# Kernel tuning notes

Measured on AMD Instinct MI355X. Metric: run time of the kernel, lower is better.

Reference implementation:

```python
import jax, jax.numpy as jnp
import numpy as np

P = 6
CUTOFF = 1.0
N_BASIS = 8
AVG_NEIGH = 16.0
NUM_LAYERS = 2
N, E, MUL, H, F = 8192, 131072, 16, 256, 16


def envelope(d):
    # polynomial cutoff u(x) with p=6 (NequIP/Allegro style)
    x = d / CUTOFF
    p = float(P)
    u = (1.0 - (p + 1.0) * (p + 2.0) / 2.0 * x ** P
         + p * (p + 2.0) * x ** (P + 1)
         - p * (p + 1.0) / 2.0 * x ** (P + 2))
    return jnp.where(x < 1.0, u, 0.0)


def bessel(d):
    k = jnp.arange(1, N_BASIS + 1, dtype=d.dtype)
    return jnp.sqrt(2.0 / CUTOFF) * jnp.sin(k[None, :] * jnp.pi * d[:, None] / CUTOFF) / d[:, None]


def sph_harm(u):
    # real spherical harmonics, ell=0..3, component normalization -> [E,16]
    x, y, z = u[:, 0], u[:, 1], u[:, 2]
    s3 = 3.0 ** 0.5
    s5 = 5.0 ** 0.5
    s15 = 15.0 ** 0.5
    s7 = 7.0 ** 0.5
    c33 = (35.0 / 8.0) ** 0.5
    c32 = 105.0 ** 0.5
    c31 = (21.0 / 8.0) ** 0.5
    one = jnp.ones_like(x)
    comps = [
        one,
        s3 * x, s3 * y, s3 * z,
        s15 * x * y, s15 * y * z, 0.5 * s5 * (3.0 * z * z - 1.0), s15 * x * z, 0.5 * s15 * (x * x - y * y),
        c33 * y * (3.0 * x * x - y * y), c32 * x * y * z, c31 * y * (5.0 * z * z - 1.0),
        0.5 * s7 * (5.0 * z ** 3 - 3.0 * z), c31 * x * (5.0 * z * z - 1.0),
        0.5 * c32 * z * (x * x - y * y), c33 * x * (x * x - 3.0 * y * y),
    ]
    return jnp.stack(comps, axis=1)


def setup_inputs() -> dict:
    key = jax.random.key(0)
    ks = jax.random.split(key, 16)
    dirs = jax.random.normal(ks[0], (E, 3), dtype=jnp.float32)
    dirs = dirs / jnp.linalg.norm(dirs, axis=1, keepdims=True)
    r = jax.random.uniform(ks[1], (E, 1), minval=0.05, maxval=0.95, dtype=jnp.float32)
    vectors = dirs * r
    node_attrs = 0.5 * jax.random.normal(ks[2], (N, F), dtype=jnp.float32)
    senders = jax.random.randint(ks[3], (E,), 0, N, dtype=jnp.int32)
    receivers = jax.random.randint(ks[4], (E,), 0, N, dtype=jnp.int32)

    def gl(k, shape):
        fan_in = shape[-2] if len(shape) >= 2 else 1
        return jax.random.normal(k, shape, dtype=jnp.float32) / jnp.sqrt(float(fan_in))

    return {
        'node_attrs': node_attrs, 'vectors': vectors,
        'senders': senders, 'receivers': receivers,
        'W_e0': gl(ks[5], (N_BASIS + 2 * F, H)), 'b_e0': jnp.zeros((H,), jnp.float32),
        'W_e1': gl(ks[6], (H, H)), 'b_e1': jnp.zeros((H,), jnp.float32),
        'W_v0': gl(ks[7], (H, MUL)),
        'W_lw': gl(ks[8], (NUM_LAYERS, H, MUL)),
        'W_lsh': gl(ks[9], (NUM_LAYERS, 16, 16)),
        'W_ly1': gl(ks[10], (NUM_LAYERS, H + MUL, H)), 'b_ly1': jnp.zeros((NUM_LAYERS, H), jnp.float32),
        'W_ly2': gl(ks[11], (NUM_LAYERS, H, H)), 'b_ly2': jnp.zeros((NUM_LAYERS, H), jnp.float32),
        'W_out': gl(ks[12], (H, 1)),
    }


def reference(node_attrs, vectors, senders, receivers, W_e0, b_e0, W_e1, b_e1, W_v0,
              W_lw, W_lsh, W_ly1, b_ly1, W_ly2, b_ly2, W_out):
    n_nodes = node_attrs.shape[0]
    inv = 1.0 / jnp.sqrt(AVG_NEIGH)
    d = jnp.linalg.norm(vectors, axis=1)                      # [E]
    u = envelope(d)                                           # [E]
    # edge embedding: radial basis + gathered endpoint attrs
    x = jnp.concatenate([bessel(d), node_attrs[senders], node_attrs[receivers]], axis=1)
    x = jax.nn.silu(x @ W_e0 + b_e0)
    x = jax.nn.silu(x @ W_e1 + b_e1)
    x = u[:, None] * x                                        # [E,H]
    Y = sph_harm(vectors / d[:, None])                        # [E,16]
    V = (x @ W_v0)[:, :, None] * Y[:, None, :]                # [E,MUL,16]
    for l in range(NUM_LAYERS):
        w = x @ W_lw[l]                                       # [E,MUL]
        wY = jax.ops.segment_sum(w[:, :, None] * Y[:, None, :], senders, num_segments=n_nodes) * inv
        wY = wY[senders]                                      # [E,MUL,16] gather back
        VV = wY * V                                           # per-edge equivariant product
        V = jnp.einsum('emi,ij->emj', VV, W_lsh[l])
        h = jnp.concatenate([x, VV[:, :, 0]], axis=1)         # scalar (l=0) channel feedback
        y = jax.nn.silu(h @ W_ly1[l] + b_ly1[l])
        y = jax.nn.silu(y @ W_ly2[l] + b_ly2[l])
        x = (x + u[:, None] * y) / jnp.sqrt(2.0)
    edge_out = (x @ W_out) * u[:, None]                       # [E,1]
    node_out = jax.ops.segment_sum(edge_out, receivers, num_segments=n_nodes) * inv
    return node_out                                           # [N,1]
```

## Files before the change

### kernel.cpp

```cpp
#include <hip/hip_runtime.h>
#include <hip/hip_bf16.h>
#include <math.h>

#define H 256
#define F 16
#define MUL 16
#define NB 8
#define LROW 296
#define YROW 264

typedef short bf16x8 __attribute__((ext_vector_type(8)));
typedef short bf16x4 __attribute__((ext_vector_type(4)));
typedef float f32x4 __attribute__((ext_vector_type(4)));
#define MFMA_B16(a, b, c) __builtin_amdgcn_mfma_f32_16x16x32_bf16(a, b, c, 0, 0, 0)

__device__ __forceinline__ float bf2f(__hip_bfloat16 x) { return __bfloat162float(x); }
__device__ __forceinline__ float silu(float x)
{
    return x * __builtin_amdgcn_rcpf(1.f + __expf(-x));
}
__device__ __forceinline__ short f2bs(float x)
{
    __hip_bfloat16 h = __float2bfloat16(x);
    short s; __builtin_memcpy(&s, &h, 2); return s;
}
__device__ __forceinline__ float bs2f(short s)
{
    __hip_bfloat16 h; __builtin_memcpy(&h, &s, 2); return __bfloat162float(h);
}
__device__ __forceinline__ float rawld(const void* p, int flag, size_t o)
{
    return flag ? ((const float*)p)[o] : bf2f(((const __hip_bfloat16*)p)[o]);
}

__global__ __launch_bounds__(256) void k_sniff(const void* vec, int* flag,
                                               int* cnt, int N)
{
    __shared__ int bad;
    int tid = threadIdx.x;
    if (tid == 0) bad = 0;
    __syncthreads();
    const __hip_bfloat16* hp = (const __hip_bfloat16*)vec;
    for (int i = tid; i < 1024; i += 256) {
        float f = bf2f(hp[i]);
        if (!(isfinite(f) && fabsf(f) <= 1.0f)) bad = 1;
    }
    for (int i = tid; i < N; i += 256) cnt[i] = 0;
    __syncthreads();
    if (tid == 0) *flag = bad;
}

struct ConvArgs {
    const void* src[7];
    float* dst[7];
    int cum[8];
};
__global__ __launch_bounds__(256) void k_conv_all(ConvArgs a, const int* __restrict__ flag,
                                                  const int* __restrict__ snd,
                                                  int* __restrict__ cnt, int E)
{
    int gid = blockIdx.x * 256 + threadIdx.x;
    if (gid < E) atomicAdd(&cnt[snd[gid]], 1);
    if (gid >= a.cum[7]) return;
    int k = 0;
    while (gid >= a.cum[k + 1]) k++;
    int i = gid - a.cum[k];
    a.dst[k][i] = rawld(a.src[k], *flag, i);
}

struct SwzArgs {
    const void* src[10];
    __hip_bfloat16* dst[10];
    int K[10], Nc[10], cum[11];
    size_t soff[10];
};
__global__ __launch_bounds__(256) void k_swz_all(SwzArgs a, const int* __restrict__ flag)
{
    int gid = blockIdx.x * 256 + threadIdx.x;
    if (gid >= a.cum[10]) return;
    int fl = *flag;
    int j = 0;
    while (gid >= a.cum[j + 1]) j++;
    int idx = gid - a.cum[j];
    int kk = idx & 31;
    int n = (idx >> 5) % a.Nc[j];
    int kt = idx / (32 * a.Nc[j]);
    int k = kt * 32 + kk;
    float v = 0.f;
    if (j == 9) {
        if (n == 0 && k < a.K[j]) v = rawld(a.src[j], fl, a.soff[j] + k);
    } else if (k < a.K[j]) {
        v = rawld(a.src[j], fl, a.soff[j] + (size_t)k * a.Nc[j] + n);
    }
    a.dst[j][idx] = __float2bfloat16(v);
}

__global__ __launch_bounds__(1024) void k_scan(const int* __restrict__ cnt,
                                               int* __restrict__ off,
                                               int* __restrict__ cur, int N)
{
    __shared__ int sums[1024];
    int tid = threadIdx.x;
    int chunk = (N + 1023) / 1024;
    int base = tid * chunk;
    int s = 0;
    for (int i = 0; i < chunk; i++) { int idx = base + i; if (idx < N) s += cnt[idx]; }
    sums[tid] = s;
    __syncthreads();
    for (int d = 1; d < 1024; d <<= 1) {
        int v = (tid >= d) ? sums[tid - d] : 0;
        __syncthreads();
        sums[tid] += v;
        __syncthreads();
    }
    int run = (tid == 0) ? 0 : sums[tid - 1];
    for (int i = 0; i < chunk; i++) {
        int idx = base + i;
        if (idx < N) { off[idx] = run; cur[idx] = run; run += cnt[idx]; }
    }
    if (tid == 1023) off[N] = run;
}

__global__ __launch_bounds__(256) void k_cscatter(const int* __restrict__ snd,
                                                  int* __restrict__ cur,
                                                  int* __restrict__ eidx, int E)
{
    int e = blockIdx.x * 256 + threadIdx.x;
    if (e >= E) return;
    int p = atomicAdd(&cur[snd[e]], 1);
    eidx[p] = e;
}


__global__ __launch_bounds__(512, 4) void k_embed_mfma(
    const float* __restrict__ vec, const float* __restrict__ na,
    const int* __restrict__ snd, const int* __restrict__ rcv,
    const __hip_bfloat16* __restrict__ We0s, const float* __restrict__ be0,
    const __hip_bfloat16* __restrict__ We1s, const float* __restrict__ be1,
    const __hip_bfloat16* __restrict__ Wv0s, const __hip_bfloat16* __restrict__ Wlws0,
    float* __restrict__ ubuf, float* __restrict__ Ybuf,
    __hip_bfloat16* __restrict__ xb, float* __restrict__ abuf,
    float* __restrict__ wbuf)
{
    __shared__ __align__(16) __hip_bfloat16 As[64 * LROW];
    __shared__ __align__(16) __hip_bfloat16 Ys[64 * YROW];
    __shared__ float us[64];
    int tid = threadIdx.x;
    int w = tid >> 6, l = tid & 63;
    int lm = l & 15, lq = l >> 4;
    int eb = blockIdx.x * 64;

    bf16x8 w0p[2][2];
#pragma unroll
    for (int kt = 0; kt < 2; kt++)
#pragma unroll
        for (int nt = 0; nt < 2; nt++)
            w0p[kt][nt] = *(const bf16x8*)(We0s + ((size_t)(kt * 256 + w * 32 + nt * 16 + lm) * 32 + lq * 8));

    {
        int el = tid & 63;
        int part = tid >> 6;
        int ge = eb + el;
        const float SQ2 = 1.41421356237309515f;
        const float PI = 3.14159265358979323846f;
        if (part == 0) {
            float vx = vec[3 * ge + 0], vy = vec[3 * ge + 1], vz = vec[3 * ge + 2];
            float d = sqrtf(vx * vx + vy * vy + vz * vz);
            float d3 = d * d * d;
            float d6 = d3 * d3, d7 = d6 * d, d8 = d7 * d;
            float u = 1.f - 28.f * d6 + 48.f * d7 - 21.f * d8;
            u = (d < 1.f) ? u : 0.f;
            ubuf[ge] = u;
            us[el] = u;
            float invd = __builtin_amdgcn_rcpf(d);
#pragma unroll
            for (int k = 1; k <= 4; k++)
                As[el * LROW + (k - 1)] = __float2bfloat16(SQ2 * __sinf((float)k * PI * d) * invd);
        } else if (part == 4) {
            float vx = vec[3 * ge + 0], vy = vec[3 * ge + 1], vz = vec[3 * ge + 2];
            float d = sqrtf(vx * vx + vy * vy + vz * vz);
            float invd = __builtin_amdgcn_rcpf(d);
#pragma unroll
            for (int k = 5; k <= 8; k++)
                As[el * LROW + (k - 1)] = __float2bfloat16(SQ2 * __sinf((float)k * PI * d) * invd);
        } else if (part == 5) {
#pragma unroll
            for (int j = 40; j < 64; j++) As[el * LROW + j] = __float2bfloat16(0.f);
        } else if (part == 1) {
            int s = snd[ge];
#pragma unroll
            for (int j = 0; j < 16; j++)
                As[el * LROW + 8 + j] = __float2bfloat16(na[(size_t)s * F + j]);
        } else if (part == 2) {
            int r = rcv[ge];
#pragma unroll
            for (int j = 0; j < 16; j++)
                As[el * LROW + 24 + j] = __float2bfloat16(na[(size_t)r * F + j]);
        } else if (part == 3) {
            float vx = vec[3 * ge + 0], vy = vec[3 * ge + 1], vz = vec[3 * ge + 2];
            float d = sqrtf(vx * vx + vy * vy + vz * vz);
            float invd = __builtin_amdgcn_rcpf(d);
            float x = vx * invd, y = vy * invd, z = vz * invd;
            const float s3 = 1.7320508075688772f;
            const float s5 = 2.2360679774997896f;
            const float s15 = 3.8729833462074170f;
            const float s7 = 2.6457513110645907f;
            const float c33 = 2.0916500663351889f;
            const float c32 = 10.246950765959598f;
            const float c31 = 1.6201851746019651f;
            float* Yp = Ybuf + (size_t)ge * 16;
            Yp[0] = 1.f;
            Yp[1] = s3 * x;  Yp[2] = s3 * y;  Yp[3] = s3 * z;
            Yp[4] = s15 * x * y;  Yp[5] = s15 * y * z;
            Yp[6] = 0.5f * s5 * (3.f * z * z - 1.f);
            Yp[7] = s15 * x * z;
            Yp[8] = 0.5f * s15 * (x * x - y * y);
            Yp[9] = c33 * y * (3.f * x * x - y * y);
            Yp[10] = c32 * x * y * z;
            Yp[11] = c31 * y * (5.f * z * z - 1.f);
            Yp[12] = 0.5f * s7 * (5.f * z * z * z - 3.f * z);
            Yp[13] = c31 * x * (5.f * z * z - 1.f);
            Yp[14] = 0.5f * c32 * z * (x * x - y * y);
            Yp[15] = c33 * x * (x * x - 3.f * y * y);
        }
    }
    __syncthreads();

    f32x4 acc[4][2];
#pragma unroll
    for (int mt = 0; mt < 4; mt++)
#pragma unroll
        for (int nt = 0; nt < 2; nt++) acc[mt][nt] = (f32x4){0.f, 0.f, 0.f, 0.f};
#pragma unroll
    for (int kt = 0; kt < 2; kt++) {
#pragma unroll
        for (int mt = 0; mt < 4; mt++) {
            bf16x8 bx = *(const bf16x8*)(As + (mt * 16 + lm) * LROW + kt * 32 + lq * 8);
#pragma unroll
            for (int nt = 0; nt < 2; nt++) acc[mt][nt] = MFMA_B16(w0p[kt][nt], bx, acc[mt][nt]);
        }
    }
    bf16x8 w1p[2][2];
#pragma unroll
    for (int kt = 0; kt < 2; kt++)
#pragma unroll
        for (int nt = 0; nt < 2; nt++)
            w1p[kt][nt] = *(const bf16x8*)(We1s + ((size_t)(kt * 256 + w * 32 + nt * 16 + lm) * 32 + lq * 8));
#pragma unroll
    for (int nt = 0; nt < 2; nt++) {
        int cb = w * 32 + nt * 16 + lq * 4;
        f32x4 bb = *(const f32x4*)(be0 + cb);
#pragma unroll
        for (int mt = 0; mt < 4; mt++) {
            int row = mt * 16 + lm;
            bf16x4 v = {f2bs(silu(acc[mt][nt][0] + bb[0])), f2bs(silu(acc[mt][nt][1] + bb[1])),
                        f2bs(silu(acc[mt][nt][2] + bb[2])), f2bs(silu(acc[mt][nt][3] + bb[3]))};
            *(bf16x4*)(Ys + row * YROW + cb) = v;
        }
    }
    __syncthreads();

#pragma unroll
    for (int mt = 0; mt < 4; mt++)
#pragma unroll
        for (int nt = 0; nt < 2; nt++) acc[mt][nt] = (f32x4){0.f, 0.f, 0.f, 0.f};
#pragma unroll
    for (int kt = 0; kt < 8; kt++) {
        bf16x8 aw[2];
#pragma unroll
        for (int nt = 0; nt < 2; nt++)
            aw[nt] = (kt < 2) ? w1p[kt][nt]
                   : *(const bf16x8*)(We1s + ((size_t)(kt * 256 + w * 32 + nt * 16 + lm) * 32 + lq * 8));
#pragma unroll
        for (int mt = 0; mt < 4; mt++) {
            bf16x8 bx = *(const bf16x8*)(Ys + (mt * 16 + lm) * YROW + kt * 32 + lq * 8);
#pragma unroll
            for (int nt = 0; nt < 2; nt++) acc[mt][nt] = MFMA_B16(aw[nt], bx, acc[mt][nt]);
        }
    }
    const __hip_bfloat16* tw = (w < 4) ? Wv0s : Wlws0;
    bf16x8 twp[2];
#pragma unroll
    for (int kt = 0; kt < 2; kt++)
        twp[kt] = *(const bf16x8*)(tw + ((size_t)(kt * 16 + lm) * 32 + lq * 8));
#pragma unroll
    for (int nt = 0; nt < 2; nt++) {
        int cb = w * 32 + nt * 16 + lq * 4;
        f32x4 bb = *(const f32x4*)(be1 + cb);
#pragma unroll
        for (int mt = 0; mt < 4; mt++) {
            int row = mt * 16 + lm;
            float uu = us[row];
            bf16x4 v = {f2bs(silu(acc[mt][nt][0] + bb[0]) * uu),
                        f2bs(silu(acc[mt][nt][1] + bb[1]) * uu),
                        f2bs(silu(acc[mt][nt][2] + bb[2]) * uu),
                        f2bs(silu(acc[mt][nt][3] + bb[3]) * uu)};
            *(bf16x4*)(As + row * LROW + cb) = v;
            *(bf16x4*)(xb + (size_t)(eb + row) * H + cb) = v;
        }
    }
    __syncthreads();

    if (w < 4) {
        f32x4 av = (f32x4){0.f, 0.f, 0.f, 0.f};
#pragma unroll
        for (int kt = 0; kt < 8; kt++) {
            bf16x8 bx = *(const bf16x8*)(As + (w * 16 + lm) * LROW + kt * 32 + lq * 8);
            bf16x8 a_v = (kt < 2) ? twp[kt]
                       : *(const bf16x8*)(Wv0s + ((size_t)(kt * 16 + lm) * 32 + lq * 8));
            av = MFMA_B16(a_v, bx, av);
        }
        *(f32x4*)(abuf + (size_t)(eb + w * 16 + lm) * 16 + lq * 4) = av;
    } else {
        int w2 = w - 4;
        f32x4 aw2 = (f32x4){0.f, 0.f, 0.f, 0.f};
#pragma unroll
        for (int kt = 0; kt < 8; kt++) {
            bf16x8 bx = *(const bf16x8*)(As + (w2 * 16 + lm) * LROW + kt * 32 + lq * 8);
            bf16x8 a_w = (kt < 2) ? twp[kt]
                       : *(const bf16x8*)(Wlws0 + ((size_t)(kt * 16 + lm) * 32 + lq * 8));
            aw2 = MFMA_B16(a_w, bx, aw2);
        }
        *(f32x4*)(wbuf + (size_t)(eb + w2 * 16 + lm) * 16 + lq * 4) = aw2;
    }
}

__global__ __launch_bounds__(256) void k_gather0(
    const int* __restrict__ off, const int* __restrict__ eidx,
    const float* __restrict__ wbuf, const float* __restrict__ Ybuf,
    const float* __restrict__ abuf,
    float* __restrict__ wYn0, __hip_bfloat16* __restrict__ vvbuf)
{
    __shared__ float ws[4][16][17];
    __shared__ float Ysh[4][16][17];
    __shared__ float w00s[4][16];
    int tid = threadIdx.x;
    int w = tid >> 6, l = tid & 63;
    int js = l >> 4, i = l & 15;
    int n0 = blockIdx.x * 4;
    int n = n0 + w;
    int beg = off[n], end = off[n + 1];
    int o0 = off[n0], o1 = off[n0 + 1], o2 = off[n0 + 2], o3 = off[n0 + 3], o4 = off[n0 + 4];
    int m01 = max(o1 - o0, o2 - o1), m23 = max(o3 - o2, o4 - o3);
    int maxc = (max(m01, m23) + 15) >> 4;
    float acc[4] = {0.f, 0.f, 0.f, 0.f};
    for (int r = 0; r < maxc; r++) {
        int c = beg + r * 16;
        int ne = min(16, end - c);
        if (ne > 0) {
#pragma unroll
            for (int k = 0; k < 4; k++) {
                int j = js + 4 * k;
                if (j < ne) {
                    int e = eidx[c + j];
                    ws[w][j][i]  = wbuf[(size_t)e * 16 + i];
                    Ysh[w][j][i] = Ybuf[(size_t)e * 16 + i];
                }
            }
        }
        __syncthreads();
        if (ne > 0) {
            for (int j2 = 0; j2 < ne; j2++) {
                float yv = Ysh[w][j2][i];
#pragma unroll
                for (int k = 0; k < 4; k++)
                    acc[k] += ws[w][j2][js + 4 * k] * yv;
            }
        }
        __syncthreads();
    }
#pragma unroll
    for (int k = 0; k < 4; k++)
        wYn0[(size_t)n * 256 + (js + 4 * k) * 16 + i] = acc[k] * 0.25f;
    if (i == 0) {
#pragma unroll
        for (int k = 0; k < 4; k++) w00s[w][js + 4 * k] = acc[k] * 0.25f;
    }
    __syncthreads();
    float w0i = w00s[w][i];
    for (int c = beg + js; c < end; c += 4) {
        int e = eidx[c];
        float a = abuf[(size_t)e * 16 + i];
        vvbuf[(size_t)e * 16 + i] = __float2bfloat16(w0i * a);
    }
}

__global__ __launch_bounds__(256) void k_gather1(
    const int* __restrict__ off, const int* __restrict__ eidx,
    const float* __restrict__ wbuf, const float* __restrict__ Ybuf,
    const float* __restrict__ abuf,
    const float* __restrict__ wYn0, const float* __restrict__ Wlsh,
    __hip_bfloat16* __restrict__ vvbuf, float* __restrict__ nacc)
{
    __shared__ float ws[4][16][17];
    __shared__ float Ysh[4][16][17];
    __shared__ float qsh[4][16][17];
    __shared__ float w10s[4][16];
    int tid = threadIdx.x;
    int w = tid >> 6, l = tid & 63;
    int js = l >> 4, i = l & 15;
    int n0 = blockIdx.x * 4;
    int n = n0 + w;
    int beg = off[n], end = off[n + 1];
    if (tid < 4) nacc[n0 + tid] = 0.f;
    int o0 = off[n0], o1 = off[n0 + 1], o2 = off[n0 + 2], o3 = off[n0 + 3], o4 = off[n0 + 4];
    int m01 = max(o1 - o0, o2 - o1), m23 = max(o3 - o2, o4 - o3);
    int maxc = (max(m01, m23) + 15) >> 4;
    float acc[4] = {0.f, 0.f, 0.f, 0.f};
    for (int r = 0; r < maxc; r++) {
        int c = beg + r * 16;
        int ne = min(16, end - c);
        if (ne > 0) {
#pragma unroll
            for (int k = 0; k < 4; k++) {
                int j = js + 4 * k;
                if (j < ne) {
                    int e = eidx[c + j];
                    ws[w][j][i]  = wbuf[(size_t)e * 16 + i];
                    Ysh[w][j][i] = Ybuf[(size_t)e * 16 + i];
                }
            }
        }
        __syncthreads();
        if (ne > 0) {
            for (int j2 = 0; j2 < ne; j2++) {
                float yv = Ysh[w][j2][i];
#pragma unroll
                for (int k = 0; k < 4; k++)
                    acc[k] += ws[w][j2][js + 4 * k] * yv;
            }
        }
        __syncthreads();
    }
    if (i == 0) {
#pragma unroll
        for (int k = 0; k < 4; k++) w10s[w][js + 4 * k] = acc[k] * 0.25f;
    }
#pragma unroll
    for (int k = 0; k < 4; k++) {
        int m = js + 4 * k;
        qsh[w][m][i] = wYn0[(size_t)n * 256 + m * 16 + i] * Wlsh[i * 16];
    }
    __syncthreads();
    float w1i = w10s[w][i];
    for (int c = beg + js; c < end; c += 4) {
        int e = eidx[c];
        float a = abuf[(size_t)e * 16 + i];
        float t = 0.f;
#pragma unroll
        for (int j = 0; j < 4; j++) {
            f32x4 yv = *(const f32x4*)(Ybuf + (size_t)e * 16 + 4 * j);
            t += qsh[w][i][4 * j + 0] * yv[0] + qsh[w][i][4 * j + 1] * yv[1]
               + qsh[w][i][4 * j + 2] * yv[2] + qsh[w][i][4 * j + 3] * yv[3];
        }
        vvbuf[(size_t)e * 16 + i] = __float2bfloat16(w1i * a * t);
    }
}

__global__ __launch_bounds__(512, 4) void k_layer_mfma(
    __hip_bfloat16* __restrict__ xb, const float* __restrict__ ubuf,
    const __hip_bfloat16* __restrict__ vvbuf, const int* __restrict__ rcv,
    const __hip_bfloat16* __restrict__ W1s, const float* __restrict__ b1,
    const __hip_bfloat16* __restrict__ W2s, const float* __restrict__ b2,
    const __hip_bfloat16* __restrict__ Wlwn, float* __restrict__ wbufn,
    const __hip_bfloat16* __restrict__ Wouts, float* __restrict__ nacc,
    int layer)
{
    __shared__ __align__(16) __hip_bfloat16 As[64 * LROW];
    __shared__ __align__(16) __hip_bfloat16 Ys[64 * YROW];
    int tid = threadIdx.x;
    int w = tid >> 6, l = tid & 63;
    int lm = l & 15, lq = l >> 4;
    int eb = blockIdx.x * 64;

    bf16x8 w1p[2][2];
#pragma unroll
    for (int kt = 0; kt < 2; kt++)
#pragma unroll
        for (int nt = 0; nt < 2; nt++)
            w1p[kt][nt] = *(const bf16x8*)(W1s + ((size_t)(kt * 256 + w * 32 + nt * 16 + lm) * 32 + lq * 8));

#pragma unroll
    for (int i = 0; i < 4; i++) {
        int c = tid + 512 * i;
        int row = c >> 5, kc = c & 31;
        *(bf16x8*)(As + row * LROW + kc * 8) =
            *(const bf16x8*)(xb + (size_t)(eb + row) * H + kc * 8);
    }
    {
        int el = tid & 63;
        int mh = (tid >> 6) * 2;
        int ge = eb + el;
        *(unsigned int*)(As + el * LROW + 256 + mh) =
            *(const unsigned int*)((const short*)vvbuf + (size_t)ge * 16 + mh);
        if (tid < 64) {
#pragma unroll
            for (int j = 0; j < 16; j++) As[tid * LROW + 272 + j] = __float2bfloat16(0.f);
        }
    }
    __syncthreads();

    float uu[4];
#pragma unroll
    for (int mt = 0; mt < 4; mt++) uu[mt] = ubuf[eb + mt * 16 + lm];

    f32x4 acc[4][2];
#pragma unroll
    for (int mt = 0; mt < 4; mt++)
#pragma unroll
        for (int nt = 0; nt < 2; nt++) acc[mt][nt] = (f32x4){0.f, 0.f, 0.f, 0.f};
#pragma unroll
    for (int kt = 0; kt < 9; kt++) {
        bf16x8 aw[2];
#pragma unroll
        for (int nt = 0; nt < 2; nt++)
            aw[nt] = (kt < 2) ? w1p[kt][nt]
                   : *(const bf16x8*)(W1s + ((size_t)(kt * 256 + w * 32 + nt * 16 + lm) * 32 + lq * 8));
#pragma unroll
        for (int mt = 0; mt < 4; mt++) {
            bf16x8 bx = *(const bf16x8*)(As + (mt * 16 + lm) * LROW + kt * 32 + lq * 8);
#pragma unroll
            for (int nt = 0; nt < 2; nt++) acc[mt][nt] = MFMA_B16(aw[nt], bx, acc[mt][nt]);
        }
    }
    bf16x8 w2p[2][2];
#pragma unroll
    for (int kt = 0; kt < 2; kt++)
#pragma unroll
        for (int nt = 0; nt < 2; nt++)
            w2p[kt][nt] = *(const bf16x8*)(W2s + ((size_t)(kt * 256 + w * 32 + nt * 16 + lm) * 32 + lq * 8));
#pragma unroll
    for (int nt = 0; nt < 2; nt++) {
        int cb = w * 32 + nt * 16 + lq * 4;
        f32x4 bb = *(const f32x4*)(b1 + cb);
#pragma unroll
        for (int mt = 0; mt < 4; mt++) {
            int row = mt * 16 + lm;
            bf16x4 v = {f2bs(silu(acc[mt][nt][0] + bb[0])), f2bs(silu(acc[mt][nt][1] + bb[1])),
                        f2bs(silu(acc[mt][nt][2] + bb[2])), f2bs(silu(acc[mt][nt][3] + bb[3]))};
            *(bf16x4*)(Ys + row * YROW + cb) = v;
        }
    }
    __syncthreads();

#pragma unroll
    for (int mt = 0; mt < 4; mt++)
#pragma unroll
        for (int nt = 0; nt < 2; nt++) acc[mt][nt] = (f32x4){0.f, 0.f, 0.f, 0.f};
#pragma unroll
    for (int kt = 0; kt < 8; kt++) {
        bf16x8 aw[2];
#pragma unroll
        for (int nt = 0; nt < 2; nt++)
            aw[nt] = (kt < 2) ? w2p[kt][nt]
                   : *(const bf16x8*)(W2s + ((size_t)(kt * 256 + w * 32 + nt * 16 + lm) * 32 + lq * 8));
#pragma unroll
        for (int mt = 0; mt < 4; mt++) {
            bf16x8 bx = *(const bf16x8*)(Ys + (mt * 16 + lm) * YROW + kt * 32 + lq * 8);
#pragma unroll
            for (int nt = 0; nt < 2; nt++) acc[mt][nt] = MFMA_B16(aw[nt], bx, acc[mt][nt]);
        }
    }
    const __hip_bfloat16* tw = (layer == 0) ? Wlwn : Wouts;
    bf16x8 twp[2];
#pragma unroll
    for (int kt = 0; kt < 2; kt++)
        twp[kt] = *(const bf16x8*)(tw + ((size_t)(kt * 16 + lm) * 32 + lq * 8));
    const float rs2 = 0.70710678118654752f;
#pragma unroll
    for (int nt = 0; nt < 2; nt++) {
        int cb = w * 32 + nt * 16 + lq * 4;
        f32x4 bb = *(const f32x4*)(b2 + cb);
#pragma unroll
        for (int mt = 0; mt < 4; mt++) {
            int row = mt * 16 + lm;
            bf16x4 xo = *(const bf16x4*)(As + row * LROW + cb);
            bf16x4 v;
#pragma unroll
            for (int r = 0; r < 4; r++) {
                float xn = (bs2f(xo[r]) + uu[mt] * silu(acc[mt][nt][r] + bb[r])) * rs2;
                v[r] = f2bs(xn);
            }
            *(bf16x4*)(As + row * LROW + cb) = v;
            if (layer == 0) *(bf16x4*)(xb + (size_t)(eb + row) * H + cb) = v;
        }
    }
    __syncthreads();

    if (layer == 0) {
        if (w < 4) {
            f32x4 cw = (f32x4){0.f, 0.f, 0.f, 0.f};
#pragma unroll
            for (int kt = 0; kt < 8; kt++) {
                bf16x8 bx = *(const bf16x8*)(As + (w * 16 + lm) * LROW + kt * 32 + lq * 8);
                bf16x8 a = (kt < 2) ? twp[kt]
                         : *(const bf16x8*)(Wlwn + ((size_t)(kt * 16 + lm) * 32 + lq * 8));
                cw = MFMA_B16(a, bx, cw);
            }
            *(f32x4*)(wbufn + (size_t)(eb + w * 16 + lm) * 16 + lq * 4) = cw;
        }
    } else {
        if (w < 4) {
            f32x4 co = (f32x4){0.f, 0.f, 0.f, 0.f};
#pragma unroll
            for (int kt = 0; kt < 8; kt++) {
                bf16x8 bx = *(const bf16x8*)(As + (w * 16 + lm) * LROW + kt * 32 + lq * 8);
                bf16x8 a = (kt < 2) ? twp[kt]
                         : *(const bf16x8*)(Wouts + ((size_t)(kt * 16 + lm) * 32 + lq * 8));
                co = MFMA_B16(a, bx, co);
            }
            if (lq == 0) {
                int e = eb + w * 16 + lm;
                atomicAdd(&nacc[rcv[e]], co[0] * ubuf[e]);
            }
        }
    }
}

__global__ __launch_bounds__(256) void k_final(
    const float* __restrict__ nacc, void* __restrict__ out, const int* __restrict__ flag,
    float inv, int N)
{
    int n = blockIdx.x * 256 + threadIdx.x;
    if (n >= N) return;
    float v = nacc[n] * inv;
    if (*flag) ((float*)out)[n] = v;
    else       ((__hip_bfloat16*)out)[n] = __float2bfloat16(v);
}

extern "C" void kernel_launch(void* const* d_in, const int* in_sizes, int n_in,
                              void* d_out, int out_size, void* d_ws, size_t ws_size,
                              hipStream_t stream)
{
    const int E = in_sizes[2];
    const int N = in_sizes[0] / F;
    (void)n_in; (void)ws_size; (void)out_size;

    char* wsb = (char*)d_ws;
    size_t off = 0;
    int* flag = (int*)wsb; off += 256;

    const int cidx[7] = {0, 1, 5, 7, 10, 12, 14};
    float* canon[7];
    for (int k = 0; k < 7; k++) {
        canon[k] = (float*)(wsb + off);
        off += (size_t)in_sizes[cidx[k]] * 4;
        off = (off + 255) & ~(size_t)255;
    }
    const float* naC   = canon[0];
    const float* vecC  = canon[1];
    const float* be0C  = canon[2];
    const float* be1C  = canon[3];
    const float* WlshC = canon[4];
    const float* bly1C = canon[5];
    const float* bly2C = canon[6];

    __hip_bfloat16* We0s  = (__hip_bfloat16*)(wsb + off); off += 64 * 256 * 2;
    __hip_bfloat16* We1s  = (__hip_bfloat16*)(wsb + off); off += 256 * 256 * 2;
    __hip_bfloat16* Wv0s  = (__hip_bfloat16*)(wsb + off); off += 256 * 16 * 2;
    __hip_bfloat16* Wlws0 = (__hip_bfloat16*)(wsb + off); off += 256 * 16 * 2;
    __hip_bfloat16* Wlws1 = (__hip_bfloat16*)(wsb + off); off += 256 * 16 * 2;
    __hip_bfloat16* W1s0  = (__hip_bfloat16*)(wsb + off); off += 288 * 256 * 2;
    __hip_bfloat16* W1s1  = (__hip_bfloat16*)(wsb + off); off += 288 * 256 * 2;
    __hip_bfloat16* W2s0  = (__hip_bfloat16*)(wsb + off); off += 256 * 256 * 2;
    __hip_bfloat16* W2s1  = (__hip_bfloat16*)(wsb + off); off += 256 * 256 * 2;
    __hip_bfloat16* Wouts = (__hip_bfloat16*)(wsb + off); off += 256 * 16 * 2;
    off = (off + 255) & ~(size_t)255;

    __hip_bfloat16* xbuf = (__hip_bfloat16*)(wsb + off); off += (size_t)E * H * 2;
    float* wYn0 = (float*)(wsb + off); off += (size_t)N * H * 4;
    __hip_bfloat16* vvbuf = (__hip_bfloat16*)(wsb + off); off += (size_t)E * 16 * 2;
    float* ubuf = (float*)(wsb + off); off += (size_t)E * 4;
    float* Ybuf = (float*)(wsb + off); off += (size_t)E * 16 * 4;
    float* abuf = (float*)(wsb + off); off += (size_t)E * 16 * 4;
    float* wbuf = (float*)(wsb + off); off += (size_t)E * 16 * 4;
    float* nacc = (float*)(wsb + off); off += (size_t)N * 4;
    int* cnt  = (int*)(wsb + off); off += (size_t)N * 4;
    int* offb = (int*)(wsb + off); off += (size_t)(N + 1) * 4;
    int* cur  = (int*)(wsb + off); off += (size_t)N * 4;
    int* eidx = (int*)(wsb + off); off += (size_t)E * 4;

    const int* snd = (const int*)d_in[2];
    const int* rcv = (const int*)d_in[3];
    const float inv = 0.25f;
    const int nb64 = E / 64;

    k_sniff<<<1, 256, 0, stream>>>(d_in[1], flag, cnt, N);
    {
        ConvArgs ca;
        int c = 0;
        for (int k = 0; k < 7; k++) {
            ca.src[k] = d_in[cidx[k]];
            ca.dst[k] = canon[k];
            ca.cum[k] = c;
            c += in_sizes[cidx[k]];
        }
        ca.cum[7] = c;
        k_conv_all<<<(c + 255) / 256, 256, 0, stream>>>(ca, flag, snd, cnt, E);
    }

    {
        SwzArgs sa;
        const void* srcs[10] = {d_in[4], d_in[6], d_in[8], d_in[9], d_in[9],
                                d_in[11], d_in[11], d_in[13], d_in[13], d_in[15]};
        size_t soffs[10]     = {0, 0, 0, 0, 256 * 16,
                                0, 272 * 256, 0, 256 * 256, 0};
        __hip_bfloat16* dsts[10] = {We0s, We1s, Wv0s, Wlws0, Wlws1,
                                    W1s0, W1s1, W2s0, W2s1, Wouts};
        int Ks[10]    = {40, 256, 256, 256, 256, 272, 272, 256, 256, 256};
        int Ncs[10]   = {256, 256, 16, 16, 16, 256, 256, 256, 256, 16};
        int Kpads[10] = {64, 256, 256, 256, 256, 288, 288, 256, 256, 256};
        int c = 0;
        for (int j = 0; j < 10; j++) {
            sa.src[j] = srcs[j]; sa.dst[j] = dsts[j];
            sa.K[j] = Ks[j]; sa.Nc[j] = Ncs[j]; sa.soff[j] = soffs[j];
            sa.cum[j] = c;
            c += (Kpads[j] >> 5) * Ncs[j] * 32;
        }
        sa.cum[10] = c;
        k_swz_all<<<(c + 255) / 256, 256, 0, stream>>>(sa, flag);
    }

    k_scan<<<1, 1024, 0, stream>>>(cnt, offb, cur, N);
    k_cscatter<<<(E + 255) / 256, 256, 0, stream>>>(snd, cur, eidx, E);

    k_embed_mfma<<<nb64, 512, 0, stream>>>(vecC, naC, snd, rcv,
                                           We0s, be0C, We1s, be1C, Wv0s, Wlws0,
                                           ubuf, Ybuf, xbuf, abuf, wbuf);

    k_gather0<<<N / 4, 256, 0, stream>>>(offb, eidx, wbuf, Ybuf, abuf, wYn0, vvbuf);
    k_layer_mfma<<<nb64, 512, 0, stream>>>(xbuf, ubuf, vvbuf, rcv,
                                           W1s0, bly1C, W2s0, bly2C,
                                           Wlws1, wbuf,
                                           (const __hip_bfloat16*)nullptr, (float*)nullptr, 0);
    k_gather1<<<N / 4, 256, 0, stream>>>(offb, eidx, wbuf, Ybuf, abuf, wYn0, WlshC,
                                         vvbuf, nacc);
    k_layer_mfma<<<nb64, 512, 0, stream>>>(xbuf, ubuf, vvbuf, rcv,
                                           W1s1, bly1C + H, W2s1, bly2C + H,
                                           (const __hip_bfloat16*)nullptr, (float*)nullptr,
                                           Wouts, nacc, 1);

    k_final<<<(N + 255) / 256, 256, 0, stream>>>(nacc, d_out, flag, inv, N);
}
```

Measured before the change: 333.1 us.

## Make layer kernel persistent over four tiles with register-prefetched next tile

Each block of the layer MLP kernel now processes four consecutive 64-edge tiles instead of one, and the grid shrinks by four. The first two k-slices of the weight fragments are loaded once per block. The next tile's x and vv rows are prefetched into registers while the current tile's MFMAs run, hiding global-load latency behind compute. The cost is more live registers, fewer blocks (512 blocks for 131072 edges), and an extra barrier per tile, which may reduce occupancy and load balance.

```diff
diff --git a/kernel.cpp b/kernel.cpp
--- a/kernel.cpp
+++ b/kernel.cpp
@@ -471,149 +471,158 @@
     int tid = threadIdx.x;
     int w = tid >> 6, l = tid & 63;
     int lm = l & 15, lq = l >> 4;
-    int eb = blockIdx.x * 64;
-
-    bf16x8 w1p[2][2];
+    int base = blockIdx.x * 4;
+
+    int srow[4], skc[4];
+#pragma unroll
+    for (int i = 0; i < 4; i++) { int c = tid + 512 * i; srow[i] = c >> 5; skc[i] = c & 31; }
+    int el = tid & 63;
+    int mh = (tid >> 6) * 2;
+
+    bf16x8 w1p[2][2], w2p[2][2], twp[2];
 #pragma unroll
     for (int kt = 0; kt < 2; kt++)
 #pragma unroll
-        for (int nt = 0; nt < 2; nt++)
+        for (int nt = 0; nt < 2; nt++) {
             w1p[kt][nt] = *(const bf16x8*)(W1s + ((size_t)(kt * 256 + w * 32 + nt * 16 + lm) * 32 + lq * 8));
-
-#pragma unroll
-    for (int i = 0; i < 4; i++) {
-        int c = tid + 512 * i;
-        int row = c >> 5, kc = c & 31;
-        *(bf16x8*)(As + row * LROW + kc * 8) =
-            *(const bf16x8*)(xb + (size_t)(eb + row) * H + kc * 8);
-    }
-    {
-        int el = tid & 63;
-        int mh = (tid >> 6) * 2;
-        int ge = eb + el;
-        *(unsigned int*)(As + el * LROW + 256 + mh) =
-            *(const unsigned int*)((const short*)vvbuf + (size_t)ge * 16 + mh);
-        if (tid < 64) {
-#pragma unroll
-            for (int j = 0; j < 16; j++) As[tid * LROW + 272 + j] = __float2bfloat16(0.f);
-        }
-    }
-    __syncthreads();
-
-    float uu[4];
-#pragma unroll
-    for (int mt = 0; mt < 4; mt++) uu[mt] = ubuf[eb + mt * 16 + lm];
-
-    f32x4 acc[4][2];
-#pragma unroll
-    for (int mt = 0; mt < 4; mt++)
-#pragma unroll
-        for (int nt = 0; nt < 2; nt++) acc[mt][nt] = (f32x4){0.f, 0.f, 0.f, 0.f};
-#pragma unroll
-    for (int kt = 0; kt < 9; kt++) {
-        bf16x8 aw[2];
-#pragma unroll
-        for (int nt = 0; nt < 2; nt++)
-            aw[nt] = (kt < 2) ? w1p[kt][nt]
-                   : *(const bf16x8*)(W1s + ((size_t)(kt * 256 + w * 32 + nt * 16 + lm) * 32 + lq * 8));
-#pragma unroll
-        for (int mt = 0; mt < 4; mt++) {
-            bf16x8 bx = *(const bf16x8*)(As + (mt * 16 + lm) * LROW + kt * 32 + lq * 8);
-#pragma unroll
-            for (int nt = 0; nt < 2; nt++) acc[mt][nt] = MFMA_B16(aw[nt], bx, acc[mt][nt]);
-        }
-    }
-    bf16x8 w2p[2][2];
-#pragma unroll
-    for (int kt = 0; kt < 2; kt++)
-#pragma unroll
-        for (int nt = 0; nt < 2; nt++)
             w2p[kt][nt] = *(const bf16x8*)(W2s + ((size_t)(kt * 256 + w * 32 + nt * 16 + lm) * 32 + lq * 8));
-#pragma unroll
-    for (int nt = 0; nt < 2; nt++) {
-        int cb = w * 32 + nt * 16 + lq * 4;
-        f32x4 bb = *(const f32x4*)(b1 + cb);
-#pragma unroll
-        for (int mt = 0; mt < 4; mt++) {
-            int row = mt * 16 + lm;
-            bf16x4 v = {f2bs(silu(acc[mt][nt][0] + bb[0])), f2bs(silu(acc[mt][nt][1] + bb[1])),
-                        f2bs(silu(acc[mt][nt][2] + bb[2])), f2bs(silu(acc[mt][nt][3] + bb[3]))};
-            *(bf16x4*)(Ys + row * YROW + cb) = v;
-        }
-    }
-    __syncthreads();
-
-#pragma unroll
-    for (int mt = 0; mt < 4; mt++)
-#pragma unroll
-        for (int nt = 0; nt < 2; nt++) acc[mt][nt] = (f32x4){0.f, 0.f, 0.f, 0.f};
-#pragma unroll
-    for (int kt = 0; kt < 8; kt++) {
-        bf16x8 aw[2];
-#pragma unroll
-        for (int nt = 0; nt < 2; nt++)
-            aw[nt] = (kt < 2) ? w2p[kt][nt]
-                   : *(const bf16x8*)(W2s + ((size_t)(kt * 256 + w * 32 + nt * 16 + lm) * 32 + lq * 8));
-#pragma unroll
-        for (int mt = 0; mt < 4; mt++) {
-            bf16x8 bx = *(const bf16x8*)(Ys + (mt * 16 + lm) * YROW + kt * 32 + lq * 8);
-#pragma unroll
-            for (int nt = 0; nt < 2; nt++) acc[mt][nt] = MFMA_B16(aw[nt], bx, acc[mt][nt]);
-        }
-    }
+        }
     const __hip_bfloat16* tw = (layer == 0) ? Wlwn : Wouts;
-    bf16x8 twp[2];
 #pragma unroll
     for (int kt = 0; kt < 2; kt++)
         twp[kt] = *(const bf16x8*)(tw + ((size_t)(kt * 16 + lm) * 32 + lq * 8));
-    const float rs2 = 0.70710678118654752f;
-#pragma unroll
-    for (int nt = 0; nt < 2; nt++) {
-        int cb = w * 32 + nt * 16 + lq * 4;
-        f32x4 bb = *(const f32x4*)(b2 + cb);
-#pragma unroll
-        for (int mt = 0; mt < 4; mt++) {
-            int row = mt * 16 + lm;
-            bf16x4 xo = *(const bf16x4*)(As + row * LROW + cb);
-            bf16x4 v;
-#pragma unroll
-            for (int r = 0; r < 4; r++) {
-                float xn = (bs2f(xo[r]) + uu[mt] * silu(acc[mt][nt][r] + bb[r])) * rs2;
-                v[r] = f2bs(xn);
-            }
-            *(bf16x4*)(As + row * LROW + cb) = v;
-            if (layer == 0) *(bf16x4*)(xb + (size_t)(eb + row) * H + cb) = v;
-        }
-    }
-    __syncthreads();
-
-    if (layer == 0) {
-        if (w < 4) {
-            f32x4 cw = (f32x4){0.f, 0.f, 0.f, 0.f};
-#pragma unroll
-            for (int kt = 0; kt < 8; kt++) {
-                bf16x8 bx = *(const bf16x8*)(As + (w * 16 + lm) * LROW + kt * 32 + lq * 8);
-                bf16x8 a = (kt < 2) ? twp[kt]
-                         : *(const bf16x8*)(Wlwn + ((size_t)(kt * 16 + lm) * 32 + lq * 8));
-                cw = MFMA_B16(a, bx, cw);
-            }
-            *(f32x4*)(wbufn + (size_t)(eb + w * 16 + lm) * 16 + lq * 4) = cw;
-        }
-    } else {
-        if (w < 4) {
-            f32x4 co = (f32x4){0.f, 0.f, 0.f, 0.f};
-#pragma unroll
-            for (int kt = 0; kt < 8; kt++) {
-                bf16x8 bx = *(const bf16x8*)(As + (w * 16 + lm) * LROW + kt * 32 + lq * 8);
-                bf16x8 a = (kt < 2) ? twp[kt]
-                         : *(const bf16x8*)(Wouts + ((size_t)(kt * 16 + lm) * 32 + lq * 8));
-                co = MFMA_B16(a, bx, co);
-            }
-            if (lq == 0) {
-                int e = eb + w * 16 + lm;
-                atomicAdd(&nacc[rcv[e]], co[0] * ubuf[e]);
-            }
-        }
+
+    bf16x8 xs[4];
+#pragma unroll
+    for (int i = 0; i < 4; i++)
+        xs[i] = *(const bf16x8*)(xb + (size_t)(base * 64 + srow[i]) * H + skc[i] * 8);
+    unsigned int vvp = *(const unsigned int*)((const short*)vvbuf + (size_t)(base * 64 + el) * 16 + mh);
+
+    for (int t = 0; t < 4; t++) {
+        int eb = (base + t) * 64;
+#pragma unroll
+        for (int i = 0; i < 4; i++)
+            *(bf16x8*)(As + srow[i] * LROW + skc[i] * 8) = xs[i];
+        *(unsigned int*)(As + el * LROW + 256 + mh) = vvp;
+        if (t == 0 && tid < 64) {
+#pragma unroll
+            for (int j = 0; j < 16; j++) As[tid * LROW + 272 + j] = __float2bfloat16(0.f);
+        }
+        __syncthreads();
+
+        if (t < 3) {
+            int ebn = (base + t + 1) * 64;
+#pragma unroll
+            for (int i = 0; i < 4; i++)
+                xs[i] = *(const bf16x8*)(xb + (size_t)(ebn + srow[i]) * H + skc[i] * 8);
+            vvp = *(const unsigned int*)((const short*)vvbuf + (size_t)(ebn + el) * 16 + mh);
+        }
+
+        float uu[4];
+#pragma unroll
+        for (int mt = 0; mt < 4; mt++) uu[mt] = ubuf[eb + mt * 16 + lm];
+
+        f32x4 acc[4][2];
+#pragma unroll
+        for (int mt = 0; mt < 4; mt++)
+#pragma unroll
+            for (int nt = 0; nt < 2; nt++) acc[mt][nt] = (f32x4){0.f, 0.f, 0.f, 0.f};
+#pragma unroll
+        for (int kt = 0; kt < 9; kt++) {
+            bf16x8 aw[2];
+#pragma unroll
+            for (int nt = 0; nt < 2; nt++)
+                aw[nt] = (kt < 2) ? w1p[kt][nt]
+                       : *(const bf16x8*)(W1s + ((size_t)(kt * 256 + w * 32 + nt * 16 + lm) * 32 + lq * 8));
+#pragma unroll
+            for (int mt = 0; mt < 4; mt++) {
+                bf16x8 bx = *(const bf16x8*)(As + (mt * 16 + lm) * LROW + kt * 32 + lq * 8);
+#pragma unroll
+                for (int nt = 0; nt < 2; nt++) acc[mt][nt] = MFMA_B16(aw[nt], bx, acc[mt][nt]);
+            }
+        }
+#pragma unroll
+        for (int nt = 0; nt < 2; nt++) {
+            int cb = w * 32 + nt * 16 + lq * 4;
+            f32x4 bb = *(const f32x4*)(b1 + cb);
+#pragma unroll
+            for (int mt = 0; mt < 4; mt++) {
+                int row = mt * 16 + lm;
+                bf16x4 v = {f2bs(silu(acc[mt][nt][0] + bb[0])), f2bs(silu(acc[mt][nt][1] + bb[1])),
+                            f2bs(silu(acc[mt][nt][2] + bb[2])), f2bs(silu(acc[mt][nt][3] + bb[3]))};
+                *(bf16x4*)(Ys + row * YROW + cb) = v;
+            }
+        }
+        __syncthreads();
+
+#pragma unroll
+        for (int mt = 0; mt < 4; mt++)
+#pragma unroll
+            for (int nt = 0; nt < 2; nt++) acc[mt][nt] = (f32x4){0.f, 0.f, 0.f, 0.f};
+#pragma unroll
+        for (int kt = 0; kt < 8; kt++) {
+            bf16x8 aw[2];
+#pragma unroll
+            for (int nt = 0; nt < 2; nt++)
+                aw[nt] = (kt < 2) ? w2p[kt][nt]
+                       : *(const bf16x8*)(W2s + ((size_t)(kt * 256 + w * 32 + nt * 16 + lm) * 32 + lq * 8));
+#pragma unroll
+            for (int mt = 0; mt < 4; mt++) {
+                bf16x8 bx = *(const bf16x8*)(Ys + (mt * 16 + lm) * YROW + kt * 32 + lq * 8);
+#pragma unroll
+                for (int nt = 0; nt < 2; nt++) acc[mt][nt] = MFMA_B16(aw[nt], bx, acc[mt][nt]);
+            }
+        }
+        const float rs2 = 0.70710678118654752f;
+#pragma unroll
+        for (int nt = 0; nt < 2; nt++) {
+            int cb = w * 32 + nt * 16 + lq * 4;
+            f32x4 bb = *(const f32x4*)(b2 + cb);
+#pragma unroll
+            for (int mt = 0; mt < 4; mt++) {
+                int row = mt * 16 + lm;
+                bf16x4 xo = *(const bf16x4*)(As + row * LROW + cb);
+                bf16x4 v;
+#pragma unroll
+                for (int r = 0; r < 4; r++) {
+                    float xn = (bs2f(xo[r]) + uu[mt] * silu(acc[mt][nt][r] + bb[r])) * rs2;
+                    v[r] = f2bs(xn);
+                }
+                *(bf16x4*)(As + row * LROW + cb) = v;
+                if (layer == 0) *(bf16x4*)(xb + (size_t)(eb + row) * H + cb) = v;
+            }
+        }
+        __syncthreads();
+
+        if (layer == 0) {
+            if (w < 4) {
+                f32x4 cw = (f32x4){0.f, 0.f, 0.f, 0.f};
+#pragma unroll
+                for (int kt = 0; kt < 8; kt++) {
+                    bf16x8 bx = *(const bf16x8*)(As + (w * 16 + lm) * LROW + kt * 32 + lq * 8);
+                    bf16x8 a = (kt < 2) ? twp[kt]
+                             : *(const bf16x8*)(Wlwn + ((size_t)(kt * 16 + lm) * 32 + lq * 8));
+                    cw = MFMA_B16(a, bx, cw);
+                }
+                *(f32x4*)(wbufn + (size_t)(eb + w * 16 + lm) * 16 + lq * 4) = cw;
+            }
+        } else {
+            if (w < 4) {
+                f32x4 co = (f32x4){0.f, 0.f, 0.f, 0.f};
+#pragma unroll
+                for (int kt = 0; kt < 8; kt++) {
+                    bf16x8 bx = *(const bf16x8*)(As + (w * 16 + lm) * LROW + kt * 32 + lq * 8);
+                    bf16x8 a = (kt < 2) ? twp[kt]
+                             : *(const bf16x8*)(Wouts + ((size_t)(kt * 16 + lm) * 32 + lq * 8));
+                    co = MFMA_B16(a, bx, co);
+                }
+                if (lq == 0) {
+                    int e = eb + w * 16 + lm;
+                    atomicAdd(&nacc[rcv[e]], co[0] * ubuf[e]);
+                }
+            }
+        }
+        __syncthreads();
     }
 }
 
@@ -729,16 +738,16 @@
                                            ubuf, Ybuf, xbuf, abuf, wbuf);
 
     k_gather0<<<N / 4, 256, 0, stream>>>(offb, eidx, wbuf, Ybuf, abuf, wYn0, vvbuf);
-    k_layer_mfma<<<nb64, 512, 0, stream>>>(xbuf, ubuf, vvbuf, rcv,
-                                           W1s0, bly1C, W2s0, bly2C,
-                                           Wlws1, wbuf,
-                                           (const __hip_bfloat16*)nullptr, (float*)nullptr, 0);
+    k_layer_mfma<<<nb64 / 4, 512, 0, stream>>>(xbuf, ubuf, vvbuf, rcv,
+                                               W1s0, bly1C, W2s0, bly2C,
+                                               Wlws1, wbuf,
+                                               (const __hip_bfloat16*)nullptr, (float*)nullptr, 0);
     k_gather1<<<N / 4, 256, 0, stream>>>(offb, eidx, wbuf, Ybuf, abuf, wYn0, WlshC,
                                          vvbuf, nacc);
-    k_layer_mfma<<<nb64, 512, 0, stream>>>(xbuf, ubuf, vvbuf, rcv,
-                                           W1s1, bly1C + H, W2s1, bly2C + H,
-                                           (const __hip_bfloat16*)nullptr, (float*)nullptr,
-                                           Wouts, nacc, 1);
+    k_layer_mfma<<<nb64 / 4, 512, 0, stream>>>(xbuf, ubuf, vvbuf, rcv,
+                                               W1s1, bly1C + H, W2s1, bly2C + H,
+                                               (const __hip_bfloat16*)nullptr, (float*)nullptr,
+                                               Wouts, nacc, 1);
 
     k_final<<<(N + 255) / 256, 256, 0, stream>>>(nacc, d_out, flag, inv, N);
 }
```

After: 586.4 us. +76.0%, slower.
